# Kernel optimization log

Hardware: AMD Instinct MI355X
Metric: run time of the kernel (lower is better)

## Reference

```python
import jax, jax.numpy as jnp
import numpy as np

GRID = 33
STRIDE = 2
HIDDEN = 256
N_LAYERS = 4
BATCH = 64
N_NODES = GRID * GRID  # 1089


def _stride_edges(g, s):
    """Replicates StrideGraphSAGE.stride_edge (including the strict j > s test)."""
    idx = np.arange(g * g).reshape(g, g)
    srcs, dsts = [], []
    # right neighbor: j < g - s
    srcs.append(idx[:, : g - s].ravel()); dsts.append(idx[:, s:].ravel())
    # down neighbor: i < g - s
    srcs.append(idx[: g - s, :].ravel()); dsts.append(idx[s:, :].ravel())
    # down-right: j < g - s and i < g - s
    srcs.append(idx[: g - s, : g - s].ravel()); dsts.append(idx[s:, s:].ravel())
    # down-left: j > s and i < g - s  (strict >, as in the original)
    srcs.append(idx[: g - s, s + 1 :].ravel()); dsts.append(idx[s:, 1 : g - s].ravel())
    return (np.concatenate(srcs).astype(np.int32),
            np.concatenate(dsts).astype(np.int32))


def setup_inputs() -> dict:
    key = jax.random.key(0)
    kx, kwl, kbl, kwr = jax.random.split(key, 4)
    x = jax.random.normal(kx, (BATCH, HIDDEN, GRID, GRID), dtype=jnp.float32)
    Wl = jax.random.normal(kwl, (N_LAYERS, HIDDEN, HIDDEN), dtype=jnp.float32) * 0.05
    bl = jax.random.normal(kbl, (N_LAYERS, HIDDEN), dtype=jnp.float32) * 0.05
    Wr = jax.random.normal(kwr, (N_LAYERS, HIDDEN, HIDDEN), dtype=jnp.float32) * 0.05
    src_np, dst_np = _stride_edges(GRID, STRIDE)
    return {
        "x": x, "Wl": Wl, "bl": bl, "Wr": Wr,
        "src": jnp.asarray(src_np), "dst": jnp.asarray(dst_np),
    }


def reference(x, Wl, bl, Wr, src, dst):
    B, C, H, W = x.shape
    N = H * W
    total = B * N
    # feature2graph: each image -> [N, C] node matrix, then batched -> [B*N, C]
    nodes = x.reshape(B, C, N).transpose(0, 2, 1).reshape(total, C)

    # The original passes the UNOFFSET single-graph edge_index to every layer,
    # so messages only flow among the first N rows; the rest get zero aggregate.
    deg = jnp.zeros((total,), x.dtype).at[dst].add(1.0)
    inv_deg = jnp.where(deg > 0, 1.0 / jnp.maximum(deg, 1.0), 0.0)[:, None]

    L = Wl.shape[0]
    outs = []
    for l in range(L):
        # SAGEConv (mean aggr): lin_l(mean_j x_src_j) + lin_r(x) ; every layer
        # is applied to the ORIGINAL node features (x is never updated).
        agg = jnp.zeros_like(nodes).at[dst].add(nodes[src]) * inv_deg
        h = agg @ Wl[l] + bl[l] + nodes @ Wr[l]
        h = jax.nn.elu(h)
        # graph2feature: raw contiguous view [N, C] -> (C, H, W) per graph
        outs.append(h.reshape(B, C, H, W))
    outs.append(x)
    return jnp.concatenate(outs, axis=1)
```

## Files before the change

### kernel.cpp

```cpp
#include <hip/hip_runtime.h>
#include <hip/hip_bf16.h>
#include <stdint.h>


#define C_DIM 256
#define GRID_G 33
#define N_NODES 1089
#define BATCH 64
#define TOTAL (BATCH * N_NODES)
#define M_PAD 69760
#define CN (C_DIM * N_NODES)
#define OUT_STRIDE_B (5 * CN)
#define NCOLS 1024
#define AGG_ROWS 1152

using bf16 = __hip_bfloat16;
typedef __attribute__((ext_vector_type(8))) short short8;
typedef __attribute__((ext_vector_type(4))) float f32x4;

#define NODES_BYTES ((size_t)M_PAD * C_DIM * 2)
#define OFF_NODES   ((size_t)0)
#define OFF_AGGB    (NODES_BYTES)
#define AGGB_BYTES  ((size_t)AGG_ROWS * C_DIM * 2)
#define OFF_WLT     (OFF_AGGB + AGGB_BYTES)
#define WT_BYTES    ((size_t)NCOLS * C_DIM * 2)
#define OFF_WRT     (OFF_WLT + WT_BYTES)

__device__ __forceinline__ void gload16(void* lds, const void* g) {
    __builtin_amdgcn_global_load_lds(
        (const __attribute__((address_space(1))) uint32_t*)g,
        (__attribute__((address_space(3))) uint32_t*)lds,
        16, 0, 0);
}

__global__ __launch_bounds__(256)
void prep_kernel(const float* __restrict__ x,
                 const float* __restrict__ Wl, const float* __restrict__ Wr,
                 bf16* __restrict__ nodes, bf16* __restrict__ WlT, bf16* __restrict__ WrT,
                 float* __restrict__ out)
{
    __shared__ char smem[33792];
    const int t = threadIdx.x;
    const int bid = blockIdx.x;
    if (bid < 128) {
        float (*tile)[65] = (float(*)[65])smem;
        const int sel = bid & 1;
        const int l = (bid >> 1) & 3;
        const int kt = ((bid >> 3) & 3) * 64;
        const int ct = ((bid >> 5) & 3) * 64;
        const float* W = sel ? Wr : Wl;
        bf16* WT = sel ? WrT : WlT;
        const int tc = t & 63;
        const int tk = t >> 6;
#pragma unroll
        for (int i = 0; i < 16; ++i) {
            int kl = i * 4 + tk;
            tile[kl][tc] = W[((size_t)(l * 256 + kt + kl)) * 256 + ct + tc];
        }
        __syncthreads();
#pragma unroll
        for (int i = 0; i < 16; ++i) {
            int cl = i * 4 + tk;
            WT[((size_t)(l * 256 + ct + cl)) * 256 + kt + tc] = __float2bfloat16(tile[tc][cl]);
        }
    } else {
        bf16 (*tile)[66] = (bf16(*)[66])smem;
        const int bid2 = bid - 128;
        const int b = bid2 / 18;
        const int n0 = (bid2 % 18) * 64;
        const int nl = t & 63;
        const int cs = t >> 6;
        const int n = n0 + nl;
        const bool nvalid = n < N_NODES;
        const float* xb = x + (size_t)b * CN;
        float* outb = out + (size_t)b * OUT_STRIDE_B + (size_t)4 * CN;
#pragma unroll 4
        for (int cc = 0; cc < 64; ++cc) {
            int c = cc * 4 + cs;
            if (nvalid) {
                float v = xb[(size_t)c * N_NODES + n];
                outb[(size_t)c * N_NODES + n] = v;
                tile[c][nl] = __float2bfloat16(v);
            }
        }
        __syncthreads();
        const int half = t >> 7;
        const int c0 = (t & 127) * 2;
#pragma unroll
        for (int it = 0; it < 32; ++it) {
            int row = it * 2 + half;
            int nr = n0 + row;
            if (nr < N_NODES) {
                __hip_bfloat162 p;
                p.x = tile[c0][row];
                p.y = tile[c0 + 1][row];
                *(__hip_bfloat162*)(nodes + ((size_t)b * N_NODES + nr) * C_DIM + c0) = p;
            }
        }
    }
}

__global__ __launch_bounds__(256)
void gather_kernel(const bf16* __restrict__ nodes, bf16* __restrict__ aggb)
{
    const int n = blockIdx.x;
    const int c = threadIdx.x;
    if (n >= N_NODES) {
        aggb[(size_t)n * C_DIM + c] = __float2bfloat16(0.f);
        return;
    }
    const int i = n / GRID_G, j = n % GRID_G;
    float s = 0.f, d = 0.f;
    if (j >= 2)           { s += __bfloat162float(nodes[(size_t)(n - 2)  * C_DIM + c]); d += 1.f; }
    if (i >= 2)           { s += __bfloat162float(nodes[(size_t)(n - 66) * C_DIM + c]); d += 1.f; }
    if (i >= 2 && j >= 2) { s += __bfloat162float(nodes[(size_t)(n - 68) * C_DIM + c]); d += 1.f; }
    if (i >= 2 && j >= 1 && j <= 30)
                          { s += __bfloat162float(nodes[(size_t)(n - 64) * C_DIM + c]); d += 1.f; }
    aggb[(size_t)n * C_DIM + c] = __float2bfloat16(d > 0.f ? s / d : 0.f);
}

__global__ __launch_bounds__(256)
void gemm_kernel(const bf16* __restrict__ nodes, const bf16* __restrict__ agg,
                 const bf16* __restrict__ WrT, const bf16* __restrict__ WlT,
                 const float* __restrict__ bias, float* __restrict__ out)
{
    __shared__ bf16 Alds[3][128 * 32];
    __shared__ bf16 Blds[3][128 * 32];
    const int t = threadIdx.x;
    const int lane = t & 63;
    const int w = t >> 6;
    const unsigned bid = blockIdx.x;
    const unsigned swz = (bid & 7) * 545 + (bid >> 3);
    const int bcol = swz & 7;
    const int brow = swz >> 3;

    f32x4 acc[4][4] = {};

    const int tq = t >> 2;
    const int kk = (((t & 3) ^ ((tq >> 1) & 3)) << 3);
    const int wr = (w >> 1) << 6;
    const int wc = (w & 1) << 6;
    const int fr = lane & 15;
    const int kq = lane >> 4;
    const int swzr = (kq ^ ((fr >> 1) & 3)) << 3;

    char* AldsB = (char*)Alds;
    char* BldsB = (char*)Blds;
    const short* AldsS = (const short*)Alds;
    const short* BldsS = (const short*)Blds;

    const int nsteps = (brow * 128 < N_NODES) ? 16 : 8;
    const bf16* Abase0 = nodes + (size_t)brow * 128 * C_DIM;
    const bf16* Abase1 = agg + (size_t)brow * 128 * C_DIM;
    const bf16* Bbase0 = WrT + (size_t)bcol * 128 * C_DIM;
    const bf16* Bbase1 = WlT + (size_t)bcol * 128 * C_DIM;

    auto STAGE = [&](int s, int buf) {
        const int k0 = (s & 7) * 32;
        const bf16* Ag = (s < 8 ? Abase0 : Abase1) + (size_t)tq * C_DIM + k0 + kk;
        const bf16* Bg = (s < 8 ? Bbase0 : Bbase1) + (size_t)tq * C_DIM + k0 + kk;
        gload16(AldsB + buf * 8192 + w * 1024,        Ag);
        gload16(AldsB + buf * 8192 + 4096 + w * 1024, Ag + 64 * C_DIM);
        gload16(BldsB + buf * 8192 + w * 1024,        Bg);
        gload16(BldsB + buf * 8192 + 4096 + w * 1024, Bg + 64 * C_DIM);
    };

    STAGE(0, 0);
    STAGE(1, 1);
    int rb = 0;
    for (int s = 0; s < nsteps; ++s) {
        if (s + 1 < nsteps) asm volatile("s_waitcnt vmcnt(4)" ::: "memory");
        else                asm volatile("s_waitcnt vmcnt(0)" ::: "memory");
        __builtin_amdgcn_s_barrier();
        if (s + 2 < nsteps) STAGE(s + 2, rb == 0 ? 2 : (rb == 1 ? 0 : 1));
        const short* Ab = AldsS + rb * 4096;
        const short* Bb = BldsS + rb * 4096;
        short8 av[4], bv[4];
#pragma unroll
        for (int m = 0; m < 4; ++m)
            av[m] = *(const short8*)(Ab + (wr + m * 16 + fr) * 32 + swzr);
#pragma unroll
        for (int n = 0; n < 4; ++n)
            bv[n] = *(const short8*)(Bb + (wc + n * 16 + fr) * 32 + swzr);
#pragma unroll
        for (int m = 0; m < 4; ++m)
#pragma unroll
            for (int n = 0; n < 4; ++n)
                acc[m][n] = __builtin_amdgcn_mfma_f32_16x16x32_bf16(
                    av[m], bv[n], acc[m][n], 0, 0, 0);
        rb = (rb == 2) ? 0 : rb + 1;
    }

    const int rq = (lane >> 4) * 4;
    const int r0 = brow * 128 + wr + rq;
    const unsigned bb0 = (unsigned)r0 / N_NODES;
    const int rsw = (int)((bb0 + 1) * N_NODES);
    const int colbase = bcol * 128 + wc + fr;
    size_t coff[4];
    float bi[4];
#pragma unroll
    for (int n = 0; n < 4; ++n) {
        int col = colbase + n * 16;
        coff[n] = (size_t)(col >> 8) * CN + (col & 255);
        bi[n] = bias[col];
    }
#pragma unroll
    for (int m = 0; m < 4; ++m) {
#pragma unroll
        for (int reg = 0; reg < 4; ++reg) {
            int r = r0 + m * 16 + reg;
            if (r < TOTAL) {
                int bb = (int)bb0 + (r >= rsw ? 1 : 0);
                int nn = r - bb * N_NODES;
                size_t base = (size_t)bb * OUT_STRIDE_B + (size_t)nn * C_DIM;
#pragma unroll
                for (int n = 0; n < 4; ++n) {
                    float v = acc[m][n][reg] + bi[n];
                    v = v > 0.f ? v : (__expf(v) - 1.0f);
                    out[base + coff[n]] = v;
                }
            }
        }
    }
}

extern "C" void kernel_launch(void* const* d_in, const int* in_sizes, int n_in,
                              void* d_out, int out_size, void* d_ws, size_t ws_size,
                              hipStream_t stream) {
    const float* x  = (const float*)d_in[0];
    const float* Wl = (const float*)d_in[1];
    const float* bl = (const float*)d_in[2];
    const float* Wr = (const float*)d_in[3];
    float* out = (float*)d_out;
    char* ws = (char*)d_ws;

    bf16* nodes = (bf16*)(ws + OFF_NODES);
    bf16* aggb  = (bf16*)(ws + OFF_AGGB);
    bf16* WlT   = (bf16*)(ws + OFF_WLT);
    bf16* WrT   = (bf16*)(ws + OFF_WRT);

    prep_kernel<<<128 + BATCH * 18, 256, 0, stream>>>(x, Wl, Wr, nodes, WlT, WrT, out);
    gather_kernel<<<AGG_ROWS, 256, 0, stream>>>(nodes, aggb);
    gemm_kernel<<<8 * 545, 256, 0, stream>>>(nodes, aggb, WrT, WlT, bl, out);
}
```

Measured before the change: 157.0 us.

## Process two column tiles per GEMM block with continuous pipeline across tiles

```diff
diff --git a/kernel.cpp b/kernel.cpp
--- a/kernel.cpp
+++ b/kernel.cpp
@@ -119,7 +119,7 @@
     aggb[(size_t)n * C_DIM + c] = __float2bfloat16(d > 0.f ? s / d : 0.f);
 }
 
-__global__ __launch_bounds__(256)
+__global__ __launch_bounds__(256, 3)
 void gemm_kernel(const bf16* __restrict__ nodes, const bf16* __restrict__ agg,
                  const bf16* __restrict__ WrT, const bf16* __restrict__ WlT,
                  const float* __restrict__ bias, float* __restrict__ out)
@@ -130,9 +130,8 @@
     const int lane = t & 63;
     const int w = t >> 6;
     const unsigned bid = blockIdx.x;
-    const unsigned swz = (bid & 7) * 545 + (bid >> 3);
-    const int bcol = swz & 7;
-    const int brow = swz >> 3;
+    const int brow = bid >> 2;
+    const int pair = bid & 3;
 
     f32x4 acc[4][4] = {};
 
@@ -149,30 +148,66 @@
     const short* AldsS = (const short*)Alds;
     const short* BldsS = (const short*)Blds;
 
-    const int nsteps = (brow * 128 < N_NODES) ? 16 : 8;
+    const int ns = (brow * 128 < N_NODES) ? 16 : 8;
+    const int totalf = ns * 2;
     const bf16* Abase0 = nodes + (size_t)brow * 128 * C_DIM;
     const bf16* Abase1 = agg + (size_t)brow * 128 * C_DIM;
-    const bf16* Bbase0 = WrT + (size_t)bcol * 128 * C_DIM;
-    const bf16* Bbase1 = WlT + (size_t)bcol * 128 * C_DIM;
-
-    auto STAGE = [&](int s, int buf) {
+
+    auto STAGE = [&](int f, int buf) {
+        const int tile = (f >= ns) ? 1 : 0;
+        const int s = f - (tile ? ns : 0);
+        const int bcol = pair * 2 + tile;
         const int k0 = (s & 7) * 32;
         const bf16* Ag = (s < 8 ? Abase0 : Abase1) + (size_t)tq * C_DIM + k0 + kk;
-        const bf16* Bg = (s < 8 ? Bbase0 : Bbase1) + (size_t)tq * C_DIM + k0 + kk;
+        const bf16* Bg = (s < 8 ? WrT : WlT) + ((size_t)(bcol * 128) + tq) * C_DIM + k0 + kk;
         gload16(AldsB + buf * 8192 + w * 1024,        Ag);
         gload16(AldsB + buf * 8192 + 4096 + w * 1024, Ag + 64 * C_DIM);
         gload16(BldsB + buf * 8192 + w * 1024,        Bg);
         gload16(BldsB + buf * 8192 + 4096 + w * 1024, Bg + 64 * C_DIM);
     };
 
+    auto EPILOGUE = [&](int bcol) {
+        const int rq = kq * 4;
+        const int r0 = brow * 128 + wr + rq;
+        const unsigned bb0 = (unsigned)r0 / N_NODES;
+        const int rsw = (int)((bb0 + 1) * N_NODES);
+        const int colbase = bcol * 128 + wc + fr;
+        size_t coff[4];
+        float bi[4];
+#pragma unroll
+        for (int n = 0; n < 4; ++n) {
+            int col = colbase + n * 16;
+            coff[n] = (size_t)(col >> 8) * CN + (col & 255);
+            bi[n] = bias[col];
+        }
+#pragma unroll
+        for (int m = 0; m < 4; ++m) {
+#pragma unroll
+            for (int reg = 0; reg < 4; ++reg) {
+                int r = r0 + m * 16 + reg;
+                if (r < TOTAL) {
+                    int bb = (int)bb0 + (r >= rsw ? 1 : 0);
+                    int nn = r - bb * N_NODES;
+                    size_t base = (size_t)bb * OUT_STRIDE_B + (size_t)nn * C_DIM;
+#pragma unroll
+                    for (int n = 0; n < 4; ++n) {
+                        float v = acc[m][n][reg] + bi[n];
+                        v = v > 0.f ? v : (__expf(v) - 1.0f);
+                        out[base + coff[n]] = v;
+                    }
+                }
+            }
+        }
+    };
+
     STAGE(0, 0);
     STAGE(1, 1);
-    int rb = 0;
-    for (int s = 0; s < nsteps; ++s) {
-        if (s + 1 < nsteps) asm volatile("s_waitcnt vmcnt(4)" ::: "memory");
+    int rb = 0, wb = 2;
+    for (int f = 0; f < totalf; ++f) {
+        if (f + 1 < totalf) asm volatile("s_waitcnt vmcnt(4)" ::: "memory");
         else                asm volatile("s_waitcnt vmcnt(0)" ::: "memory");
         __builtin_amdgcn_s_barrier();
-        if (s + 2 < nsteps) STAGE(s + 2, rb == 0 ? 2 : (rb == 1 ? 0 : 1));
+        if (f + 2 < totalf) STAGE(f + 2, wb);
         const short* Ab = AldsS + rb * 4096;
         const short* Bb = BldsS + rb * 4096;
         short8 av[4], bv[4];
@@ -188,40 +223,18 @@
             for (int n = 0; n < 4; ++n)
                 acc[m][n] = __builtin_amdgcn_mfma_f32_16x16x32_bf16(
                     av[m], bv[n], acc[m][n], 0, 0, 0);
+        if (f == ns - 1) {
+            EPILOGUE(pair * 2);
+#pragma unroll
+            for (int m = 0; m < 4; ++m)
+#pragma unroll
+                for (int n = 0; n < 4; ++n)
+                    acc[m][n] = (f32x4){0.f, 0.f, 0.f, 0.f};
+        }
         rb = (rb == 2) ? 0 : rb + 1;
+        wb = (wb == 2) ? 0 : wb + 1;
     }
-
-    const int rq = (lane >> 4) * 4;
-    const int r0 = brow * 128 + wr + rq;
-    const unsigned bb0 = (unsigned)r0 / N_NODES;
-    const int rsw = (int)((bb0 + 1) * N_NODES);
-    const int colbase = bcol * 128 + wc + fr;
-    size_t coff[4];
-    float bi[4];
-#pragma unroll
-    for (int n = 0; n < 4; ++n) {
-        int col = colbase + n * 16;
-        coff[n] = (size_t)(col >> 8) * CN + (col & 255);
-        bi[n] = bias[col];
-    }
-#pragma unroll
-    for (int m = 0; m < 4; ++m) {
-#pragma unroll
-        for (int reg = 0; reg < 4; ++reg) {
-            int r = r0 + m * 16 + reg;
-            if (r < TOTAL) {
-                int bb = (int)bb0 + (r >= rsw ? 1 : 0);
-                int nn = r - bb * N_NODES;
-                size_t base = (size_t)bb * OUT_STRIDE_B + (size_t)nn * C_DIM;
-#pragma unroll
-                for (int n = 0; n < 4; ++n) {
-                    float v = acc[m][n][reg] + bi[n];
-                    v = v > 0.f ? v : (__expf(v) - 1.0f);
-                    out[base + coff[n]] = v;
-                }
-            }
-        }
-    }
+    EPILOGUE(pair * 2 + 1);
 }
 
 extern "C" void kernel_launch(void* const* d_in, const int* in_sizes, int n_in,
@@ -241,5 +254,5 @@
 
     prep_kernel<<<128 + BATCH * 18, 256, 0, stream>>>(x, Wl, Wr, nodes, WlT, WrT, out);
     gather_kernel<<<AGG_ROWS, 256, 0, stream>>>(nodes, aggb);
-    gemm_kernel<<<8 * 545, 256, 0, stream>>>(nodes, aggb, WrT, WlT, bl, out);
-}
+    gemm_kernel<<<545 * 4, 256, 0, stream>>>(nodes, aggb, WrT, WlT, bl, out);
+}
```

Result: slower. 208.1 us (+32.6%).

## Make GEMM persistent with balanced row-tile jobs per block and cross-job prefetch

Applied to the files above, without the earlier changes.

```diff
diff --git a/kernel.cpp b/kernel.cpp
--- a/kernel.cpp
+++ b/kernel.cpp
@@ -130,9 +130,13 @@
     const int lane = t & 63;
     const int w = t >> 6;
     const unsigned bid = blockIdx.x;
-    const unsigned swz = (bid & 7) * 545 + (bid >> 3);
-    const int bcol = swz & 7;
-    const int brow = swz >> 3;
+    const int j6 = (int)(bid >> 3);
+    const int bcol = j6 / 12;
+    const int s = (int)(bid & 7) * 12 + (j6 - bcol * 12);
+    const int T = (s < 65) ? 6 : 5;
+    const bool mix = (s < 9);
+    const int nj = T + (mix ? 1 : 0);
+    const int totalf = nj * 8;
 
     f32x4 acc[4][4] = {};
 
@@ -149,77 +153,109 @@
     const short* AldsS = (const short*)Alds;
     const short* BldsS = (const short*)Blds;
 
-    const int nsteps = (brow * 128 < N_NODES) ? 16 : 8;
-    const bf16* Abase0 = nodes + (size_t)brow * 128 * C_DIM;
-    const bf16* Abase1 = agg + (size_t)brow * 128 * C_DIM;
-    const bf16* Bbase0 = WrT + (size_t)bcol * 128 * C_DIM;
-    const bf16* Bbase1 = WlT + (size_t)bcol * 128 * C_DIM;
-
-    auto STAGE = [&](int s, int buf) {
-        const int k0 = (s & 7) * 32;
-        const bf16* Ag = (s < 8 ? Abase0 : Abase1) + (size_t)tq * C_DIM + k0 + kk;
-        const bf16* Bg = (s < 8 ? Bbase0 : Bbase1) + (size_t)tq * C_DIM + k0 + kk;
+    auto jobBrow = [&](int j) { int jg = mix ? (j <= 1 ? 0 : j - 1) : j; return s + 96 * jg; };
+    auto jobA = [&](int j) -> const bf16* {
+        const bf16* sa = (mix && j == 1) ? agg : nodes;
+        return sa + ((size_t)jobBrow(j) * 128 + tq) * C_DIM + kk;
+    };
+    auto jobB = [&](int j) -> const bf16* {
+        const bf16* sb = (mix && j == 1) ? WlT : WrT;
+        return sb + ((size_t)bcol * 128 + tq) * C_DIM + kk;
+    };
+
+    auto stage4 = [&](const bf16* Ag, const bf16* Bg, int buf) {
         gload16(AldsB + buf * 8192 + w * 1024,        Ag);
         gload16(AldsB + buf * 8192 + 4096 + w * 1024, Ag + 64 * C_DIM);
         gload16(BldsB + buf * 8192 + w * 1024,        Bg);
         gload16(BldsB + buf * 8192 + 4096 + w * 1024, Bg + 64 * C_DIM);
     };
 
-    STAGE(0, 0);
-    STAGE(1, 1);
+    auto EPILOGUE = [&](int brw) {
+        const int rq = kq * 4;
+        const int r0 = brw * 128 + wr + rq;
+        const unsigned bb0 = (unsigned)r0 / N_NODES;
+        const int rsw = (int)((bb0 + 1) * N_NODES);
+        const int colbase = bcol * 128 + wc + fr;
+        size_t coff[4];
+        float bi[4];
+#pragma unroll
+        for (int n = 0; n < 4; ++n) {
+            int col = colbase + n * 16;
+            coff[n] = (size_t)(col >> 8) * CN + (col & 255);
+            bi[n] = bias[col];
+        }
+#pragma unroll
+        for (int m = 0; m < 4; ++m) {
+#pragma unroll
+            for (int reg = 0; reg < 4; ++reg) {
+                int r = r0 + m * 16 + reg;
+                if (r < TOTAL) {
+                    int bb = (int)bb0 + (r >= rsw ? 1 : 0);
+                    int nn = r - bb * N_NODES;
+                    size_t base = (size_t)bb * OUT_STRIDE_B + (size_t)nn * C_DIM;
+#pragma unroll
+                    for (int n = 0; n < 4; ++n) {
+                        float v = acc[m][n][reg] + bi[n];
+                        v = v > 0.f ? v : (__expf(v) - 1.0f);
+                        out[base + coff[n]] = v;
+                    }
+                }
+            }
+        }
+    };
+
+    {
+        const bf16* A0 = jobA(0);
+        const bf16* B0 = jobB(0);
+        stage4(A0,      B0,      0);
+        stage4(A0 + 32, B0 + 32, 1);
+    }
     int rb = 0;
-    for (int s = 0; s < nsteps; ++s) {
-        if (s + 1 < nsteps) asm volatile("s_waitcnt vmcnt(4)" ::: "memory");
-        else                asm volatile("s_waitcnt vmcnt(0)" ::: "memory");
-        __builtin_amdgcn_s_barrier();
-        if (s + 2 < nsteps) STAGE(s + 2, rb == 0 ? 2 : (rb == 1 ? 0 : 1));
-        const short* Ab = AldsS + rb * 4096;
-        const short* Bb = BldsS + rb * 4096;
-        short8 av[4], bv[4];
-#pragma unroll
-        for (int m = 0; m < 4; ++m)
-            av[m] = *(const short8*)(Ab + (wr + m * 16 + fr) * 32 + swzr);
-#pragma unroll
-        for (int n = 0; n < 4; ++n)
-            bv[n] = *(const short8*)(Bb + (wc + n * 16 + fr) * 32 + swzr);
-#pragma unroll
-        for (int m = 0; m < 4; ++m)
+    bool prevEpi = false;
+    for (int j = 0; j < nj; ++j) {
+        const bf16* curA = jobA(j);
+        const bf16* curB = jobB(j);
+        const int fbase = j * 8;
+#pragma unroll
+        for (int ss = 0; ss < 8; ++ss) {
+            const int f = fbase + ss;
+            if (ss == 0 && prevEpi)     asm volatile("s_waitcnt vmcnt(0)" ::: "memory");
+            else if (f + 1 < totalf)    asm volatile("s_waitcnt vmcnt(4)" ::: "memory");
+            else                        asm volatile("s_waitcnt vmcnt(0)" ::: "memory");
+            __builtin_amdgcn_s_barrier();
+            if (f + 2 < totalf) {
+                const int wb = rb == 0 ? 2 : (rb == 1 ? 0 : 1);
+                if (ss < 6)       stage4(curA + (ss + 2) * 32, curB + (ss + 2) * 32, wb);
+                else if (ss == 6) stage4(jobA(j + 1),      jobB(j + 1),      wb);
+                else              stage4(jobA(j + 1) + 32, jobB(j + 1) + 32, wb);
+            }
+            const short* Ab = AldsS + rb * 4096;
+            const short* Bb = BldsS + rb * 4096;
+            short8 av[4], bv[4];
+#pragma unroll
+            for (int m = 0; m < 4; ++m)
+                av[m] = *(const short8*)(Ab + (wr + m * 16 + fr) * 32 + swzr);
 #pragma unroll
             for (int n = 0; n < 4; ++n)
-                acc[m][n] = __builtin_amdgcn_mfma_f32_16x16x32_bf16(
-                    av[m], bv[n], acc[m][n], 0, 0, 0);
-        rb = (rb == 2) ? 0 : rb + 1;
-    }
-
-    const int rq = (lane >> 4) * 4;
-    const int r0 = brow * 128 + wr + rq;
-    const unsigned bb0 = (unsigned)r0 / N_NODES;
-    const int rsw = (int)((bb0 + 1) * N_NODES);
-    const int colbase = bcol * 128 + wc + fr;
-    size_t coff[4];
-    float bi[4];
-#pragma unroll
-    for (int n = 0; n < 4; ++n) {
-        int col = colbase + n * 16;
-        coff[n] = (size_t)(col >> 8) * CN + (col & 255);
-        bi[n] = bias[col];
-    }
-#pragma unroll
-    for (int m = 0; m < 4; ++m) {
-#pragma unroll
-        for (int reg = 0; reg < 4; ++reg) {
-            int r = r0 + m * 16 + reg;
-            if (r < TOTAL) {
-                int bb = (int)bb0 + (r >= rsw ? 1 : 0);
-                int nn = r - bb * N_NODES;
-                size_t base = (size_t)bb * OUT_STRIDE_B + (size_t)nn * C_DIM;
-#pragma unroll
-                for (int n = 0; n < 4; ++n) {
-                    float v = acc[m][n][reg] + bi[n];
-                    v = v > 0.f ? v : (__expf(v) - 1.0f);
-                    out[base + coff[n]] = v;
-                }
-            }
+                bv[n] = *(const short8*)(Bb + (wc + n * 16 + fr) * 32 + swzr);
+#pragma unroll
+            for (int m = 0; m < 4; ++m)
+#pragma unroll
+                for (int n = 0; n < 4; ++n)
+                    acc[m][n] = __builtin_amdgcn_mfma_f32_16x16x32_bf16(
+                        av[m], bv[n], acc[m][n], 0, 0, 0);
+            rb = (rb == 2) ? 0 : rb + 1;
+        }
+        if (!(mix && j == 0)) {
+            EPILOGUE(jobBrow(j));
+#pragma unroll
+            for (int m = 0; m < 4; ++m)
+#pragma unroll
+                for (int n = 0; n < 4; ++n)
+                    acc[m][n] = (f32x4){0.f, 0.f, 0.f, 0.f};
+            prevEpi = true;
+        } else {
+            prevEpi = false;
         }
     }
 }
@@ -241,5 +277,5 @@
 
     prep_kernel<<<128 + BATCH * 18, 256, 0, stream>>>(x, Wl, Wr, nodes, WlT, WrT, out);
     gather_kernel<<<AGG_ROWS, 256, 0, stream>>>(nodes, aggb);
-    gemm_kernel<<<8 * 545, 256, 0, stream>>>(nodes, aggb, WrT, WlT, bl, out);
-}
+    gemm_kernel<<<768, 256, 0, stream>>>(nodes, aggb, WrT, WlT, bl, out);
+}
```

Result: slower. 194.3 us (+23.8%).
